# Performance work log

Measured on AMD Instinct MI355X. Metric: run time of the kernel, lower is better.

Reference implementation:

```python
import jax, jax.numpy as jnp
import numpy as np

B, S, H = 1, 2048, 2880
NH, HD = 64, 64            # num_attention_heads, head_dim
NKV = 8                    # num_key_value_heads
GROUPS = NH // NKV         # 8
RANK = 384                 # kv_lora_rank
ROPE_BASE = 150000.0
NEG = -3.4e38              # additive mask value (finfo min-ish)


def setup_inputs() -> dict:
    key = jax.random.key(0)
    ks = jax.random.split(key, 8)
    init = 0.02
    hidden_states = jax.random.normal(ks[0], (B, S, H), dtype=jnp.float32)
    # causal additive mask [B,1,S,S]
    causal = jnp.tril(jnp.ones((S, S), dtype=bool))
    attention_mask = jnp.where(causal, 0.0, NEG).astype(jnp.float32)[None, None]
    attention_mask = jnp.broadcast_to(attention_mask, (B, 1, S, S))
    q_w = jax.random.normal(ks[1], (NH * HD, H), dtype=jnp.float32) * init
    q_b = jnp.zeros((NH * HD,), dtype=jnp.float32)
    kv_a_w = jax.random.normal(ks[2], (RANK, H), dtype=jnp.float32) * init
    kv_b_w = jax.random.normal(ks[3], (NKV * HD * 2, RANK), dtype=jnp.float32) * init
    o_w = jax.random.normal(ks[4], (H, NH * HD), dtype=jnp.float32) * init
    o_b = jnp.zeros((H,), dtype=jnp.float32)
    return {"hidden_states": hidden_states, "attention_mask": attention_mask,
            "q_w": q_w, "q_b": q_b, "kv_a_w": kv_a_w, "kv_b_w": kv_b_w,
            "o_w": o_w, "o_b": o_b}


def _rotate_half(x):
    x1, x2 = x[..., : x.shape[-1] // 2], x[..., x.shape[-1] // 2:]
    return jnp.concatenate((-x2, x1), axis=-1)


def _rope_cos_sin(S, dtype):
    inv_freq = 1.0 / (ROPE_BASE ** (jnp.arange(0, HD, 2, dtype=jnp.float32) / HD))
    pos = jnp.arange(S, dtype=jnp.float32)
    freqs = pos[:, None] * inv_freq[None, :]          # [S, HD/2]
    emb = jnp.concatenate((freqs, freqs), axis=-1)    # [S, HD]
    # [1, 1, S, HD] to broadcast over batch and heads
    return jnp.cos(emb).astype(dtype)[None, None], jnp.sin(emb).astype(dtype)[None, None]


def reference(hidden_states, attention_mask, q_w, q_b, kv_a_w, kv_b_w, o_w, o_b):
    B, S, H = hidden_states.shape
    # Q projection -> [B, NH, S, HD]
    q = (hidden_states @ q_w.T + q_b).reshape(B, S, NH, HD).transpose(0, 2, 1, 3)
    # compressed KV -> decompress
    compressed_kv = hidden_states @ kv_a_w.T                 # [B, S, RANK]
    kv = (compressed_kv @ kv_b_w.T).reshape(B, S, NKV, 2 * HD)
    k, v = kv[..., :HD], kv[..., HD:]
    k = k.transpose(0, 2, 1, 3)                              # [B, NKV, S, HD]
    v = v.transpose(0, 2, 1, 3)
    # full-dim RoPE (module applies rotary over entire head_dim)
    cos, sin = _rope_cos_sin(S, q.dtype)
    q = q * cos + _rotate_half(q) * sin
    k = k * cos + _rotate_half(k) * sin
    # GQA expand: repeat_interleave over head axis
    k = jnp.repeat(k, GROUPS, axis=1)                        # [B, NH, S, HD]
    v = jnp.repeat(v, GROUPS, axis=1)
    scores = jnp.einsum('bhqd,bhkd->bhqk', q, k) / np.sqrt(HD)
    scores = scores + attention_mask
    probs = jax.nn.softmax(scores.astype(jnp.float32), axis=-1).astype(q.dtype)
    attn = jnp.einsum('bhqk,bhkd->bhqd', probs, v)           # [B, NH, S, HD]
    attn = attn.transpose(0, 2, 1, 3).reshape(B, S, NH * HD)
    return attn @ o_w.T + o_b
```

## Files before the change

### kernel.cpp

```cpp
#include <hip/hip_runtime.h>
#include <math.h>

typedef unsigned short u16;
typedef unsigned int u32;
typedef float f4 __attribute__((ext_vector_type(4)));
typedef short bf16x8 __attribute__((ext_vector_type(8)));
typedef float f32x4 __attribute__((ext_vector_type(4)));

#define S_LEN 2048
#define H_DIM 2880
#define NQD 4096
#define RANKD 384
#define HD 64
#define NH 64
#define NKV 8
#define RLN 0.37244970541f
#define LOG2E 1.4426950408889634f

__device__ __forceinline__ u16 f2bf(float f) {
  u32 u = __float_as_uint(f);
  u += 0x7fffu + ((u >> 16) & 1u);
  return (u16)(u >> 16);
}

#define GLOAD_LDS(g, l) __builtin_amdgcn_global_load_lds( \
    (__attribute__((address_space(1))) void*)(g),          \
    (__attribute__((address_space(3))) void*)(l), 16, 0, 0)

__device__ __forceinline__ size_t koff_s(int s) {
  return (size_t)((s >> 6) * 4096 + ((s >> 4) & 3) * 1024 + (s & 15) * 8);
}
__device__ __forceinline__ int koff_d(int d) {
  return (d >> 5) * 512 + ((d >> 3) & 3) * 128 + (d & 7);
}
__device__ __forceinline__ size_t voff_s(int s) {
  return (size_t)((s >> 6) * 4096 + ((s >> 5) & 1) * 512 + ((s >> 3) & 3) * 128 + (s & 7));
}
__device__ __forceinline__ int voff_d(int d) {
  return ((d >> 4) & 3) * 1024 + (d & 15) * 8;
}

__global__ void conv_f2b(const float* __restrict__ in, u16* __restrict__ out, int n4) {
  int i = blockIdx.x * blockDim.x + threadIdx.x;
  if (i >= n4) return;
  f4 v = ((const f4*)in)[i];
  ushort4 o;
  o.x = f2bf(v[0]); o.y = f2bf(v[1]); o.z = f2bf(v[2]); o.w = f2bf(v[3]);
  ((ushort4*)out)[i] = o;
}

__global__ __launch_bounds__(256) void gemm128(
    const u16* __restrict__ A, const u16* __restrict__ W,
    const float* __restrict__ bias, int K,
    u16* __restrict__ out0) {
  __shared__ __align__(16) u16 As[2 * 2 * 128 * 32];
  __shared__ __align__(16) u16 Bs[2 * 2 * 128 * 32];
  int t = threadIdx.x, w = t >> 6, L = t & 63;
  int lm = L & 15, quad = L >> 4;
  int m0 = blockIdx.x * 128, n0 = blockIdx.y * 128;
  int wm = w >> 1, wn = w & 1;
  int srow = L >> 2, scol8 = (L & 3) * 8;
  const u16* Ag0 = A + (size_t)(m0 + (w * 2) * 16 + srow) * K + scol8;
  const u16* Ag1 = Ag0 + (size_t)16 * K;
  const u16* Wg0 = W + (size_t)(n0 + (w * 2) * 16 + srow) * K + scol8;
  const u16* Wg1 = Wg0 + (size_t)16 * K;
  u16* lA0 = &As[(w * 2) * 512];
  u16* lA1 = &As[(w * 2 + 1) * 512];
  u16* lB0 = &Bs[(w * 2) * 512];
  u16* lB1 = &Bs[(w * 2 + 1) * 512];
  f32x4 acc[4][4] = {};
  int nk = K >> 6;
  GLOAD_LDS(Ag0, lA0);           GLOAD_LDS(Ag1, lA1);
  GLOAD_LDS(Ag0 + 32, lA0 + 4096); GLOAD_LDS(Ag1 + 32, lA1 + 4096);
  GLOAD_LDS(Wg0, lB0);           GLOAD_LDS(Wg1, lB1);
  GLOAD_LDS(Wg0 + 32, lB0 + 4096); GLOAD_LDS(Wg1 + 32, lB1 + 4096);
  Ag0 += 64; Ag1 += 64; Wg0 += 64; Wg1 += 64;
  __syncthreads();
  for (int kt = 0; kt < nk; ++kt) {
    int cur = (kt & 1) << 13;
    int nxt = 8192 - cur;
    if (kt + 1 < nk) {
      GLOAD_LDS(Ag0, lA0 + nxt);           GLOAD_LDS(Ag1, lA1 + nxt);
      GLOAD_LDS(Ag0 + 32, lA0 + nxt + 4096); GLOAD_LDS(Ag1 + 32, lA1 + nxt + 4096);
      GLOAD_LDS(Wg0, lB0 + nxt);           GLOAD_LDS(Wg1, lB1 + nxt);
      GLOAD_LDS(Wg0 + 32, lB0 + nxt + 4096); GLOAD_LDS(Wg1 + 32, lB1 + nxt + 4096);
      Ag0 += 64; Ag1 += 64; Wg0 += 64; Wg1 += 64;
    }
#pragma unroll
    for (int h = 0; h < 2; ++h) {
      int base = cur + h * 4096;
      bf16x8 af[4], bf[4];
#pragma unroll
      for (int i = 0; i < 4; ++i) af[i] = *(const bf16x8*)&As[base + (wm * 64 + i * 16 + lm) * 32 + quad * 8];
#pragma unroll
      for (int j = 0; j < 4; ++j) bf[j] = *(const bf16x8*)&Bs[base + (wn * 64 + j * 16 + lm) * 32 + quad * 8];
#pragma unroll
      for (int i = 0; i < 4; ++i)
#pragma unroll
        for (int j = 0; j < 4; ++j)
          acc[i][j] = __builtin_amdgcn_mfma_f32_16x16x32_bf16(af[i], bf[j], acc[i][j], 0, 0, 0);
    }
    __syncthreads();
  }
  int head = (n0 + wn * 64) >> 6;
  float b0v = bias[head * 64 + lm];
  float b1v = bias[head * 64 + 16 + lm];
  float b2v = bias[head * 64 + 32 + lm];
  float b3v = bias[head * 64 + 48 + lm];
  float invf1 = __expf(-(float)lm * RLN);
  float invf2 = __expf(-(float)(lm + 16) * RLN);
#pragma unroll
  for (int i = 0; i < 4; ++i) {
    int sq = m0 + wm * 64 + i * 16 + quad * 4;
#pragma unroll
    for (int r = 0; r < 4; ++r) {
      float a0 = acc[i][0][r] + b0v, a1 = acc[i][1][r] + b1v;
      float a2 = acc[i][2][r] + b2v, a3 = acc[i][3][r] + b3v;
      float s1, c1, s2, c2;
      sincosf((float)(sq + r) * invf1, &s1, &c1);
      sincosf((float)(sq + r) * invf2, &s2, &c2);
      u16* op = out0 + ((size_t)head * S_LEN + sq + r) * HD;
      op[lm]      = f2bf((a0 * c1 - a2 * s1) * 0.125f);
      op[lm + 32] = f2bf((a2 * c1 + a0 * s1) * 0.125f);
      op[lm + 16] = f2bf((a1 * c2 - a3 * s2) * 0.125f);
      op[lm + 48] = f2bf((a3 * c2 + a1 * s2) * 0.125f);
    }
  }
}

__global__ __launch_bounds__(256) void gemm64(
    const u16* __restrict__ A, const u16* __restrict__ W,
    const float* __restrict__ bias, int K, int Nreal,
    float* __restrict__ out) {
  __shared__ __align__(16) u16 As[2 * 2 * 64 * 32];
  __shared__ __align__(16) u16 Bs[2 * 2 * 128 * 32];
  int t = threadIdx.x, w = t >> 6, L = t & 63;
  int lm = L & 15, quad = L >> 4;
  int m0 = blockIdx.x * 64, n0 = blockIdx.y * 128;
  int wm = w >> 1, wn = w & 1;
  int srow = L >> 2, scol8 = (L & 3) * 8;
  const u16* Ag = A + (size_t)(m0 + w * 16 + srow) * K + scol8;
  int wr0 = n0 + w * 16 + srow;      if (wr0 > Nreal - 1) wr0 = Nreal - 1;
  int wr1 = n0 + 64 + w * 16 + srow; if (wr1 > Nreal - 1) wr1 = Nreal - 1;
  const u16* Wg0 = W + (size_t)wr0 * K + scol8;
  const u16* Wg1 = W + (size_t)wr1 * K + scol8;
  u16* lA  = &As[w * 512];
  u16* lB0 = &Bs[w * 512];
  u16* lB1 = &Bs[2048 + w * 512];
  f32x4 acc[2][4] = {};
  int nk = K >> 6;
  GLOAD_LDS(Ag, lA);            GLOAD_LDS(Ag + 32, lA + 2048);
  GLOAD_LDS(Wg0, lB0);          GLOAD_LDS(Wg0 + 32, lB0 + 4096);
  GLOAD_LDS(Wg1, lB1);          GLOAD_LDS(Wg1 + 32, lB1 + 4096);
  Ag += 64; Wg0 += 64; Wg1 += 64;
  __syncthreads();
  for (int kt = 0; kt < nk; ++kt) {
    int curA = (kt & 1) << 12;
    int curB = (kt & 1) << 13;
    int nxtA = 4096 - curA, nxtB = 8192 - curB;
    if (kt + 1 < nk) {
      GLOAD_LDS(Ag, lA + nxtA);          GLOAD_LDS(Ag + 32, lA + nxtA + 2048);
      GLOAD_LDS(Wg0, lB0 + nxtB);        GLOAD_LDS(Wg0 + 32, lB0 + nxtB + 4096);
      GLOAD_LDS(Wg1, lB1 + nxtB);        GLOAD_LDS(Wg1 + 32, lB1 + nxtB + 4096);
      Ag += 64; Wg0 += 64; Wg1 += 64;
    }
#pragma unroll
    for (int h = 0; h < 2; ++h) {
      int baseA = curA + h * 2048;
      int baseB = curB + h * 4096;
      bf16x8 af[2], bf[4];
#pragma unroll
      for (int i = 0; i < 2; ++i) af[i] = *(const bf16x8*)&As[baseA + (wm * 32 + i * 16 + lm) * 32 + quad * 8];
#pragma unroll
      for (int j = 0; j < 4; ++j) bf[j] = *(const bf16x8*)&Bs[baseB + (wn * 64 + j * 16 + lm) * 32 + quad * 8];
#pragma unroll
      for (int i = 0; i < 2; ++i)
#pragma unroll
        for (int j = 0; j < 4; ++j)
          acc[i][j] = __builtin_amdgcn_mfma_f32_16x16x32_bf16(af[i], bf[j], acc[i][j], 0, 0, 0);
    }
    __syncthreads();
  }
#pragma unroll
  for (int i = 0; i < 2; ++i) {
#pragma unroll
    for (int r = 0; r < 4; ++r) {
      int row = m0 + wm * 32 + i * 16 + quad * 4 + r;
#pragma unroll
      for (int j = 0; j < 4; ++j) {
        int col = n0 + wn * 64 + j * 16 + lm;
        if (col < Nreal)
          out[(size_t)row * Nreal + col] = acc[i][j][r] + bias[col];
      }
    }
  }
}

__global__ __launch_bounds__(256) void gemm_bt(
    const u16* __restrict__ A, const u16* __restrict__ W,
    int M, int N, int K, int mode,
    u16* __restrict__ out0, u16* __restrict__ out1) {
  __shared__ __align__(16) u16 As[64 * 32];
  __shared__ __align__(16) u16 Bs[64 * 32];
  int t = threadIdx.x;
  int m0 = blockIdx.x * 64, n0 = blockIdx.y * 64;
  int w = t >> 6, L = t & 63;
  int srow = t >> 2, scol = (t & 3) * 8;
  int lm = L & 15, quad = L >> 4;
  const u16* Ap = A + (size_t)(m0 + srow) * K + scol;
  const u16* Wp = W + (size_t)(n0 + srow) * K + scol;
  f32x4 acc0 = {0.f, 0.f, 0.f, 0.f}, acc1 = acc0, acc2 = acc0, acc3 = acc0;
  int aoff = (w * 16 + lm) * 32 + quad * 8;
  int boff = lm * 32 + quad * 8;
  int nk = K >> 5;
  uint4 av = *(const uint4*)Ap;
  uint4 wv = *(const uint4*)Wp;
  for (int kt = 0; kt < nk; ++kt) {
    *(uint4*)&As[srow * 32 + scol] = av;
    *(uint4*)&Bs[srow * 32 + scol] = wv;
    __syncthreads();
    if (kt + 1 < nk) {
      Ap += 32; Wp += 32;
      av = *(const uint4*)Ap;
      wv = *(const uint4*)Wp;
    }
    bf16x8 af = *(const bf16x8*)&As[aoff];
    bf16x8 b0 = *(const bf16x8*)&Bs[boff];
    bf16x8 b1 = *(const bf16x8*)&Bs[boff + 16 * 32];
    bf16x8 b2 = *(const bf16x8*)&Bs[boff + 32 * 32];
    bf16x8 b3 = *(const bf16x8*)&Bs[boff + 48 * 32];
    acc0 = __builtin_amdgcn_mfma_f32_16x16x32_bf16(af, b0, acc0, 0, 0, 0);
    acc1 = __builtin_amdgcn_mfma_f32_16x16x32_bf16(af, b1, acc1, 0, 0, 0);
    acc2 = __builtin_amdgcn_mfma_f32_16x16x32_bf16(af, b2, acc2, 0, 0, 0);
    acc3 = __builtin_amdgcn_mfma_f32_16x16x32_bf16(af, b3, acc3, 0, 0, 0);
    __syncthreads();
  }
  int mbase = m0 + w * 16 + quad * 4;
  if (mode == 3) {
    for (int r = 0; r < 4; ++r) {
      int row = mbase + r;
      float vals[4] = {acc0[r], acc1[r], acc2[r], acc3[r]};
      for (int nt = 0; nt < 4; ++nt)
        out0[(size_t)row * N + (n0 + nt * 16 + lm)] = f2bf(vals[nt]);
    }
  } else {
    bool isV = ((blockIdx.y & 1) == 1);
    int head = (n0 >> 7);
    size_t hb = (size_t)head << 17;
    if (isV) {
      int dof[4];
#pragma unroll
      for (int nt = 0; nt < 4; ++nt) dof[nt] = voff_d(nt * 16 + lm);
      for (int r = 0; r < 4; ++r) {
        int s = mbase + r;
        size_t so = hb + voff_s(s);
        float vals[4] = {acc0[r], acc1[r], acc2[r], acc3[r]};
#pragma unroll
        for (int nt = 0; nt < 4; ++nt)
          out1[so + dof[nt]] = f2bf(vals[nt]);
      }
    } else {
      int d0 = koff_d(lm), d1 = koff_d(lm + 16), d2 = koff_d(lm + 32), d3 = koff_d(lm + 48);
      float invf1 = __expf(-(float)lm * RLN);
      float invf2 = __expf(-(float)(lm + 16) * RLN);
      for (int r = 0; r < 4; ++r) {
        int s = mbase + r;
        float a0 = acc0[r], a1 = acc1[r], a2 = acc2[r], a3 = acc3[r];
        float s1, c1, s2, c2;
        sincosf((float)s * invf1, &s1, &c1);
        sincosf((float)s * invf2, &s2, &c2);
        s1 *= LOG2E; c1 *= LOG2E; s2 *= LOG2E; c2 *= LOG2E;
        size_t so = hb + koff_s(s);
        out0[so + d0] = f2bf(a0 * c1 - a2 * s1);
        out0[so + d2] = f2bf(a2 * c1 + a0 * s1);
        out0[so + d1] = f2bf(a1 * c2 - a3 * s2);
        out0[so + d3] = f2bf(a3 * c2 + a1 * s2);
      }
    }
  }
}

__global__ __launch_bounds__(256, 4) void attn_v3(
    const u16* __restrict__ Qb, const u16* __restrict__ Kf,
    const u16* __restrict__ Vf, u16* __restrict__ attnb) {
  __shared__ __align__(16) u16 Ps[4 * 16 * 72];
  int t = threadIdx.x;
  int w = t >> 6, L = t & 63;
  int lm = L & 15, quad = L >> 4;
  int h = blockIdx.x, qt = blockIdx.y, kvh = h >> 3;
  u16* pw = &Ps[w * 16 * 72];
  const u16* Kbase = Kf + ((size_t)kvh << 17) + L * 8;
  const u16* Vbase = Vf + ((size_t)kvh << 17) + L * 8;

  int q0 = qt * 64;
  const u16* Qp = Qb + ((size_t)h * S_LEN + q0 + w * 16 + lm) * HD + quad * 8;
  bf16x8 qf0 = *(const bf16x8*)Qp;
  bf16x8 qf1 = *(const bf16x8*)(Qp + 32);
  f32x4 o[4] = {};
  float m_ = -3.0e38f, l_ = 0.f;

  for (int c = 0; c <= qt; ++c) {
    const u16* Kc = Kbase + (size_t)c * 4096;
    bf16x8 kfa[4], kfb[4];
#pragma unroll
    for (int j = 0; j < 4; ++j) {
      kfa[j] = *(const bf16x8*)(Kc + j * 1024);
      kfb[j] = *(const bf16x8*)(Kc + j * 1024 + 512);
    }
    f32x4 st[4] = {};
    __builtin_amdgcn_s_setprio(1);
#pragma unroll
    for (int j = 0; j < 4; ++j) {
      st[j] = __builtin_amdgcn_mfma_f32_16x16x32_bf16(kfa[j], qf0, st[j], 0, 0, 0);
      st[j] = __builtin_amdgcn_mfma_f32_16x16x32_bf16(kfb[j], qf1, st[j], 0, 0, 0);
    }
    __builtin_amdgcn_s_setprio(0);
    const u16* Vc = Vbase + (size_t)c * 4096;
    bf16x8 vfa[4], vfb[4];
#pragma unroll
    for (int j = 0; j < 4; ++j) {
      vfa[j] = *(const bf16x8*)(Vc + j * 1024);
      vfb[j] = *(const bf16x8*)(Vc + j * 1024 + 512);
    }
    if (c == qt) {
      int qloc = w * 16 + lm;
#pragma unroll
      for (int j = 0; j < 4; ++j) {
        int kvb = j * 16 + quad * 4;
#pragma unroll
        for (int r = 0; r < 4; ++r)
          if (kvb + r > qloc) st[j][r] = -3.0e38f;
      }
    }
    float mloc = -3.0e38f;
#pragma unroll
    for (int j = 0; j < 4; ++j)
      mloc = fmaxf(mloc, fmaxf(fmaxf(st[j][0], st[j][1]), fmaxf(st[j][2], st[j][3])));
    mloc = fmaxf(mloc, __shfl_xor(mloc, 16));
    mloc = fmaxf(mloc, __shfl_xor(mloc, 32));
    float mn;
    if (__all(mloc - m_ <= 11.0f)) {
      mn = m_;
    } else {
      mn = fmaxf(m_, mloc);
      float al = exp2f(m_ - mn);
      m_ = mn;
      l_ *= al;
      float a0 = __shfl(al, quad * 4 + 0);
      float a1 = __shfl(al, quad * 4 + 1);
      float a2 = __shfl(al, quad * 4 + 2);
      float a3 = __shfl(al, quad * 4 + 3);
#pragma unroll
      for (int j = 0; j < 4; ++j) {
        o[j][0] *= a0; o[j][1] *= a1; o[j][2] *= a2; o[j][3] *= a3;
      }
    }
    float sum = 0.f;
    u16* pws = pw + lm * 72;
#pragma unroll
    for (int j = 0; j < 4; ++j) {
      float p0 = exp2f(st[j][0] - mn);
      float p1 = exp2f(st[j][1] - mn);
      float p2 = exp2f(st[j][2] - mn);
      float p3 = exp2f(st[j][3] - mn);
      sum += (p0 + p1) + (p2 + p3);
      uint2 pk;
      asm("v_cvt_pk_bf16_f32 %0, %1, %2" : "=v"(pk.x) : "v"(p0), "v"(p1));
      asm("v_cvt_pk_bf16_f32 %0, %1, %2" : "=v"(pk.y) : "v"(p2), "v"(p3));
      *(uint2*)(pws + j * 16 + quad * 4) = pk;
    }
    l_ += sum;
    bf16x8 pa = *(const bf16x8*)(pw + lm * 72 + quad * 8);
    bf16x8 pb = *(const bf16x8*)(pw + lm * 72 + 32 + quad * 8);
    __builtin_amdgcn_s_setprio(1);
#pragma unroll
    for (int j = 0; j < 4; ++j) {
      o[j] = __builtin_amdgcn_mfma_f32_16x16x32_bf16(pa, vfa[j], o[j], 0, 0, 0);
      o[j] = __builtin_amdgcn_mfma_f32_16x16x32_bf16(pb, vfb[j], o[j], 0, 0, 0);
    }
    __builtin_amdgcn_s_setprio(0);
  }
  l_ += __shfl_xor(l_, 16);
  l_ += __shfl_xor(l_, 32);
  float linv = 1.0f / l_;
  float li0 = __shfl(linv, quad * 4 + 0);
  float li1 = __shfl(linv, quad * 4 + 1);
  float li2 = __shfl(linv, quad * 4 + 2);
  float li3 = __shfl(linv, quad * 4 + 3);
#pragma unroll
  for (int r = 0; r < 4; ++r) {
    float lr = (r == 0) ? li0 : (r == 1) ? li1 : (r == 2) ? li2 : li3;
    int row = q0 + w * 16 + quad * 4 + r;
    u16* op = attnb + (size_t)row * NQD + h * HD;
    op[lm]      = f2bf(o[0][r] * lr);
    op[lm + 16] = f2bf(o[1][r] * lr);
    op[lm + 32] = f2bf(o[2][r] * lr);
    op[lm + 48] = f2bf(o[3][r] * lr);
  }
}

extern "C" void kernel_launch(void* const* d_in, const int* in_sizes, int n_in,
                              void* d_out, int out_size, void* d_ws, size_t ws_size,
                              hipStream_t stream) {
  (void)in_sizes; (void)n_in; (void)out_size; (void)ws_size;
  const float* hidden = (const float*)d_in[0];
  const float* q_w    = (const float*)d_in[2];
  const float* q_b    = (const float*)d_in[3];
  const float* kv_a_w = (const float*)d_in[4];
  const float* kv_b_w = (const float*)d_in[5];
  const float* o_w    = (const float*)d_in[6];
  const float* o_b    = (const float*)d_in[7];

  char* ws = (char*)d_ws;
  u16* hb    = (u16*)(ws + 0);
  u16* qwb   = (u16*)(ws + 11796480);
  u16* kab   = (u16*)(ws + 35389440);
  u16* kbb   = (u16*)(ws + 37601280);
  u16* owb   = (u16*)(ws + 38387712);
  u16* Qb    = (u16*)(ws + 61980672);
  u16* CKVb  = (u16*)(ws + 78757888);
  u16* Kfb   = (u16*)(ws + 80330752);
  u16* Vfb   = (u16*)(ws + 82427904);
  u16* attnb = (u16*)(ws + 84525056);

  conv_f2b<<<(1474560 + 255) / 256, 256, 0, stream>>>(hidden, hb, 1474560);
  conv_f2b<<<(2949120 + 255) / 256, 256, 0, stream>>>(q_w, qwb, 2949120);
  conv_f2b<<<(276480 + 255) / 256, 256, 0, stream>>>(kv_a_w, kab, 276480);
  conv_f2b<<<(98304 + 255) / 256, 256, 0, stream>>>(kv_b_w, kbb, 98304);
  conv_f2b<<<(2949120 + 255) / 256, 256, 0, stream>>>(o_w, owb, 2949120);

  gemm128<<<dim3(16, 32), 256, 0, stream>>>(hb, qwb, q_b, H_DIM, Qb);
  gemm_bt<<<dim3(32, 6),  256, 0, stream>>>(hb, kab, S_LEN, RANKD, H_DIM, 3, CKVb, nullptr);
  gemm_bt<<<dim3(32, 16), 256, 0, stream>>>(CKVb, kbb, S_LEN, 1024, RANKD, 2, Kfb, Vfb);
  attn_v3<<<dim3(64, 32), 256, 0, stream>>>(Qb, Kfb, Vfb, attnb);
  gemm64<<<dim3(32, 23), 256, 0, stream>>>(attnb, owb, o_b, NQD, H_DIM, (float*)d_out);
}
```

Baseline: 417.7 us.

## Pair causal q-tiles per attention block and double-buffer gemm_bt via direct LDS loads

The attention kernel now processes two query tiles per block, qt and 31-qt, so every block gets a roughly equal amount of causal work, and the grid is halved. The small projection GEMM switches to global-to-LDS direct loads with a double-buffered 64-wide K step, to hide load latency and cut VGPR staging. The trade-offs are fewer blocks in flight for attention and reliance on the async LDS loads being complete at each barrier.

```diff
diff --git a/kernel.cpp b/kernel.cpp
--- a/kernel.cpp
+++ b/kernel.cpp
@@ -200,39 +200,46 @@
     const u16* __restrict__ A, const u16* __restrict__ W,
     int M, int N, int K, int mode,
     u16* __restrict__ out0, u16* __restrict__ out1) {
-  __shared__ __align__(16) u16 As[64 * 32];
-  __shared__ __align__(16) u16 Bs[64 * 32];
+  __shared__ __align__(16) u16 As[2 * 2 * 64 * 32];
+  __shared__ __align__(16) u16 Bs[2 * 2 * 64 * 32];
   int t = threadIdx.x;
   int m0 = blockIdx.x * 64, n0 = blockIdx.y * 64;
   int w = t >> 6, L = t & 63;
-  int srow = t >> 2, scol = (t & 3) * 8;
   int lm = L & 15, quad = L >> 4;
-  const u16* Ap = A + (size_t)(m0 + srow) * K + scol;
-  const u16* Wp = W + (size_t)(n0 + srow) * K + scol;
+  int srow = w * 16 + (L >> 2), scol = (L & 3) * 8;
+  const u16* Ag = A + (size_t)(m0 + srow) * K + scol;
+  const u16* Wg = W + (size_t)(n0 + srow) * K + scol;
+  u16* lA = &As[w * 512];
+  u16* lB = &Bs[w * 512];
   f32x4 acc0 = {0.f, 0.f, 0.f, 0.f}, acc1 = acc0, acc2 = acc0, acc3 = acc0;
   int aoff = (w * 16 + lm) * 32 + quad * 8;
   int boff = lm * 32 + quad * 8;
-  int nk = K >> 5;
-  uint4 av = *(const uint4*)Ap;
-  uint4 wv = *(const uint4*)Wp;
+  int nk = K >> 6;
+  GLOAD_LDS(Ag, lA);       GLOAD_LDS(Ag + 32, lA + 2048);
+  GLOAD_LDS(Wg, lB);       GLOAD_LDS(Wg + 32, lB + 2048);
+  Ag += 64; Wg += 64;
+  __syncthreads();
   for (int kt = 0; kt < nk; ++kt) {
-    *(uint4*)&As[srow * 32 + scol] = av;
-    *(uint4*)&Bs[srow * 32 + scol] = wv;
-    __syncthreads();
+    int cur = (kt & 1) << 12;
+    int nxt = 4096 - cur;
     if (kt + 1 < nk) {
-      Ap += 32; Wp += 32;
-      av = *(const uint4*)Ap;
-      wv = *(const uint4*)Wp;
-    }
-    bf16x8 af = *(const bf16x8*)&As[aoff];
-    bf16x8 b0 = *(const bf16x8*)&Bs[boff];
-    bf16x8 b1 = *(const bf16x8*)&Bs[boff + 16 * 32];
-    bf16x8 b2 = *(const bf16x8*)&Bs[boff + 32 * 32];
-    bf16x8 b3 = *(const bf16x8*)&Bs[boff + 48 * 32];
-    acc0 = __builtin_amdgcn_mfma_f32_16x16x32_bf16(af, b0, acc0, 0, 0, 0);
-    acc1 = __builtin_amdgcn_mfma_f32_16x16x32_bf16(af, b1, acc1, 0, 0, 0);
-    acc2 = __builtin_amdgcn_mfma_f32_16x16x32_bf16(af, b2, acc2, 0, 0, 0);
-    acc3 = __builtin_amdgcn_mfma_f32_16x16x32_bf16(af, b3, acc3, 0, 0, 0);
+      GLOAD_LDS(Ag, lA + nxt);   GLOAD_LDS(Ag + 32, lA + nxt + 2048);
+      GLOAD_LDS(Wg, lB + nxt);   GLOAD_LDS(Wg + 32, lB + nxt + 2048);
+      Ag += 64; Wg += 64;
+    }
+#pragma unroll
+    for (int hh = 0; hh < 2; ++hh) {
+      int base = cur + hh * 2048;
+      bf16x8 af = *(const bf16x8*)&As[base + aoff];
+      bf16x8 b0 = *(const bf16x8*)&Bs[base + boff];
+      bf16x8 b1 = *(const bf16x8*)&Bs[base + boff + 16 * 32];
+      bf16x8 b2 = *(const bf16x8*)&Bs[base + boff + 32 * 32];
+      bf16x8 b3 = *(const bf16x8*)&Bs[base + boff + 48 * 32];
+      acc0 = __builtin_amdgcn_mfma_f32_16x16x32_bf16(af, b0, acc0, 0, 0, 0);
+      acc1 = __builtin_amdgcn_mfma_f32_16x16x32_bf16(af, b1, acc1, 0, 0, 0);
+      acc2 = __builtin_amdgcn_mfma_f32_16x16x32_bf16(af, b2, acc2, 0, 0, 0);
+      acc3 = __builtin_amdgcn_mfma_f32_16x16x32_bf16(af, b3, acc3, 0, 0, 0);
+    }
     __syncthreads();
   }
   int mbase = m0 + w * 16 + quad * 4;
@@ -287,115 +294,118 @@
   int t = threadIdx.x;
   int w = t >> 6, L = t & 63;
   int lm = L & 15, quad = L >> 4;
-  int h = blockIdx.x, qt = blockIdx.y, kvh = h >> 3;
+  int bx = blockIdx.x, h = blockIdx.y, kvh = h >> 3;
   u16* pw = &Ps[w * 16 * 72];
   const u16* Kbase = Kf + ((size_t)kvh << 17) + L * 8;
   const u16* Vbase = Vf + ((size_t)kvh << 17) + L * 8;
 
-  int q0 = qt * 64;
-  const u16* Qp = Qb + ((size_t)h * S_LEN + q0 + w * 16 + lm) * HD + quad * 8;
-  bf16x8 qf0 = *(const bf16x8*)Qp;
-  bf16x8 qf1 = *(const bf16x8*)(Qp + 32);
-  f32x4 o[4] = {};
-  float m_ = -3.0e38f, l_ = 0.f;
-
-  for (int c = 0; c <= qt; ++c) {
-    const u16* Kc = Kbase + (size_t)c * 4096;
-    bf16x8 kfa[4], kfb[4];
-#pragma unroll
-    for (int j = 0; j < 4; ++j) {
-      kfa[j] = *(const bf16x8*)(Kc + j * 1024);
-      kfb[j] = *(const bf16x8*)(Kc + j * 1024 + 512);
-    }
-    f32x4 st[4] = {};
-    __builtin_amdgcn_s_setprio(1);
-#pragma unroll
-    for (int j = 0; j < 4; ++j) {
-      st[j] = __builtin_amdgcn_mfma_f32_16x16x32_bf16(kfa[j], qf0, st[j], 0, 0, 0);
-      st[j] = __builtin_amdgcn_mfma_f32_16x16x32_bf16(kfb[j], qf1, st[j], 0, 0, 0);
-    }
-    __builtin_amdgcn_s_setprio(0);
-    const u16* Vc = Vbase + (size_t)c * 4096;
-    bf16x8 vfa[4], vfb[4];
-#pragma unroll
-    for (int j = 0; j < 4; ++j) {
-      vfa[j] = *(const bf16x8*)(Vc + j * 1024);
-      vfb[j] = *(const bf16x8*)(Vc + j * 1024 + 512);
-    }
-    if (c == qt) {
-      int qloc = w * 16 + lm;
-#pragma unroll
-      for (int j = 0; j < 4; ++j) {
-        int kvb = j * 16 + quad * 4;
-#pragma unroll
-        for (int r = 0; r < 4; ++r)
-          if (kvb + r > qloc) st[j][r] = -3.0e38f;
-      }
-    }
-    float mloc = -3.0e38f;
-#pragma unroll
-    for (int j = 0; j < 4; ++j)
-      mloc = fmaxf(mloc, fmaxf(fmaxf(st[j][0], st[j][1]), fmaxf(st[j][2], st[j][3])));
-    mloc = fmaxf(mloc, __shfl_xor(mloc, 16));
-    mloc = fmaxf(mloc, __shfl_xor(mloc, 32));
-    float mn;
-    if (__all(mloc - m_ <= 11.0f)) {
-      mn = m_;
-    } else {
-      mn = fmaxf(m_, mloc);
-      float al = exp2f(m_ - mn);
-      m_ = mn;
-      l_ *= al;
-      float a0 = __shfl(al, quad * 4 + 0);
-      float a1 = __shfl(al, quad * 4 + 1);
-      float a2 = __shfl(al, quad * 4 + 2);
-      float a3 = __shfl(al, quad * 4 + 3);
-#pragma unroll
-      for (int j = 0; j < 4; ++j) {
-        o[j][0] *= a0; o[j][1] *= a1; o[j][2] *= a2; o[j][3] *= a3;
-      }
-    }
-    float sum = 0.f;
-    u16* pws = pw + lm * 72;
-#pragma unroll
-    for (int j = 0; j < 4; ++j) {
-      float p0 = exp2f(st[j][0] - mn);
-      float p1 = exp2f(st[j][1] - mn);
-      float p2 = exp2f(st[j][2] - mn);
-      float p3 = exp2f(st[j][3] - mn);
-      sum += (p0 + p1) + (p2 + p3);
-      uint2 pk;
-      asm("v_cvt_pk_bf16_f32 %0, %1, %2" : "=v"(pk.x) : "v"(p0), "v"(p1));
-      asm("v_cvt_pk_bf16_f32 %0, %1, %2" : "=v"(pk.y) : "v"(p2), "v"(p3));
-      *(uint2*)(pws + j * 16 + quad * 4) = pk;
-    }
-    l_ += sum;
-    bf16x8 pa = *(const bf16x8*)(pw + lm * 72 + quad * 8);
-    bf16x8 pb = *(const bf16x8*)(pw + lm * 72 + 32 + quad * 8);
-    __builtin_amdgcn_s_setprio(1);
-#pragma unroll
-    for (int j = 0; j < 4; ++j) {
-      o[j] = __builtin_amdgcn_mfma_f32_16x16x32_bf16(pa, vfa[j], o[j], 0, 0, 0);
-      o[j] = __builtin_amdgcn_mfma_f32_16x16x32_bf16(pb, vfb[j], o[j], 0, 0, 0);
-    }
-    __builtin_amdgcn_s_setprio(0);
-  }
-  l_ += __shfl_xor(l_, 16);
-  l_ += __shfl_xor(l_, 32);
-  float linv = 1.0f / l_;
-  float li0 = __shfl(linv, quad * 4 + 0);
-  float li1 = __shfl(linv, quad * 4 + 1);
-  float li2 = __shfl(linv, quad * 4 + 2);
-  float li3 = __shfl(linv, quad * 4 + 3);
-#pragma unroll
-  for (int r = 0; r < 4; ++r) {
-    float lr = (r == 0) ? li0 : (r == 1) ? li1 : (r == 2) ? li2 : li3;
-    int row = q0 + w * 16 + quad * 4 + r;
-    u16* op = attnb + (size_t)row * NQD + h * HD;
-    op[lm]      = f2bf(o[0][r] * lr);
-    op[lm + 16] = f2bf(o[1][r] * lr);
-    op[lm + 32] = f2bf(o[2][r] * lr);
-    op[lm + 48] = f2bf(o[3][r] * lr);
+  for (int ph = 0; ph < 2; ++ph) {
+    int qt = ph ? (31 - bx) : bx;
+    int q0 = qt * 64;
+    const u16* Qp = Qb + ((size_t)h * S_LEN + q0 + w * 16 + lm) * HD + quad * 8;
+    bf16x8 qf0 = *(const bf16x8*)Qp;
+    bf16x8 qf1 = *(const bf16x8*)(Qp + 32);
+    f32x4 o[4] = {};
+    float m_ = -3.0e38f, l_ = 0.f;
+
+    for (int c = 0; c <= qt; ++c) {
+      const u16* Kc = Kbase + (size_t)c * 4096;
+      bf16x8 kfa[4], kfb[4];
+#pragma unroll
+      for (int j = 0; j < 4; ++j) {
+        kfa[j] = *(const bf16x8*)(Kc + j * 1024);
+        kfb[j] = *(const bf16x8*)(Kc + j * 1024 + 512);
+      }
+      f32x4 st[4] = {};
+      __builtin_amdgcn_s_setprio(1);
+#pragma unroll
+      for (int j = 0; j < 4; ++j) {
+        st[j] = __builtin_amdgcn_mfma_f32_16x16x32_bf16(kfa[j], qf0, st[j], 0, 0, 0);
+        st[j] = __builtin_amdgcn_mfma_f32_16x16x32_bf16(kfb[j], qf1, st[j], 0, 0, 0);
+      }
+      __builtin_amdgcn_s_setprio(0);
+      const u16* Vc = Vbase + (size_t)c * 4096;
+      bf16x8 vfa[4], vfb[4];
+#pragma unroll
+      for (int j = 0; j < 4; ++j) {
+        vfa[j] = *(const bf16x8*)(Vc + j * 1024);
+        vfb[j] = *(const bf16x8*)(Vc + j * 1024 + 512);
+      }
+      if (c == qt) {
+        int qloc = w * 16 + lm;
+#pragma unroll
+        for (int j = 0; j < 4; ++j) {
+          int kvb = j * 16 + quad * 4;
+#pragma unroll
+          for (int r = 0; r < 4; ++r)
+            if (kvb + r > qloc) st[j][r] = -3.0e38f;
+        }
+      }
+      float mloc = -3.0e38f;
+#pragma unroll
+      for (int j = 0; j < 4; ++j)
+        mloc = fmaxf(mloc, fmaxf(fmaxf(st[j][0], st[j][1]), fmaxf(st[j][2], st[j][3])));
+      mloc = fmaxf(mloc, __shfl_xor(mloc, 16));
+      mloc = fmaxf(mloc, __shfl_xor(mloc, 32));
+      float mn;
+      if (__all(mloc - m_ <= 11.0f)) {
+        mn = m_;
+      } else {
+        mn = fmaxf(m_, mloc);
+        float al = exp2f(m_ - mn);
+        m_ = mn;
+        l_ *= al;
+        float a0 = __shfl(al, quad * 4 + 0);
+        float a1 = __shfl(al, quad * 4 + 1);
+        float a2 = __shfl(al, quad * 4 + 2);
+        float a3 = __shfl(al, quad * 4 + 3);
+#pragma unroll
+        for (int j = 0; j < 4; ++j) {
+          o[j][0] *= a0; o[j][1] *= a1; o[j][2] *= a2; o[j][3] *= a3;
+        }
+      }
+      float sum = 0.f;
+      u16* pws = pw + lm * 72;
+#pragma unroll
+      for (int j = 0; j < 4; ++j) {
+        float p0 = exp2f(st[j][0] - mn);
+        float p1 = exp2f(st[j][1] - mn);
+        float p2 = exp2f(st[j][2] - mn);
+        float p3 = exp2f(st[j][3] - mn);
+        sum += (p0 + p1) + (p2 + p3);
+        uint2 pk;
+        asm("v_cvt_pk_bf16_f32 %0, %1, %2" : "=v"(pk.x) : "v"(p0), "v"(p1));
+        asm("v_cvt_pk_bf16_f32 %0, %1, %2" : "=v"(pk.y) : "v"(p2), "v"(p3));
+        *(uint2*)(pws + j * 16 + quad * 4) = pk;
+      }
+      l_ += sum;
+      bf16x8 pa = *(const bf16x8*)(pw + lm * 72 + quad * 8);
+      bf16x8 pb = *(const bf16x8*)(pw + lm * 72 + 32 + quad * 8);
+      __builtin_amdgcn_s_setprio(1);
+#pragma unroll
+      for (int j = 0; j < 4; ++j) {
+        o[j] = __builtin_amdgcn_mfma_f32_16x16x32_bf16(pa, vfa[j], o[j], 0, 0, 0);
+        o[j] = __builtin_amdgcn_mfma_f32_16x16x32_bf16(pb, vfb[j], o[j], 0, 0, 0);
+      }
+      __builtin_amdgcn_s_setprio(0);
+    }
+    l_ += __shfl_xor(l_, 16);
+    l_ += __shfl_xor(l_, 32);
+    float linv = 1.0f / l_;
+    float li0 = __shfl(linv, quad * 4 + 0);
+    float li1 = __shfl(linv, quad * 4 + 1);
+    float li2 = __shfl(linv, quad * 4 + 2);
+    float li3 = __shfl(linv, quad * 4 + 3);
+#pragma unroll
+    for (int r = 0; r < 4; ++r) {
+      float lr = (r == 0) ? li0 : (r == 1) ? li1 : (r == 2) ? li2 : li3;
+      int row = q0 + w * 16 + quad * 4 + r;
+      u16* op = attnb + (size_t)row * NQD + h * HD;
+      op[lm]      = f2bf(o[0][r] * lr);
+      op[lm + 16] = f2bf(o[1][r] * lr);
+      op[lm + 32] = f2bf(o[2][r] * lr);
+      op[lm + 48] = f2bf(o[3][r] * lr);
+    }
   }
 }
 
@@ -432,6 +442,6 @@
   gemm128<<<dim3(16, 32), 256, 0, stream>>>(hb, qwb, q_b, H_DIM, Qb);
   gemm_bt<<<dim3(32, 6),  256, 0, stream>>>(hb, kab, S_LEN, RANKD, H_DIM, 3, CKVb, nullptr);
   gemm_bt<<<dim3(32, 16), 256, 0, stream>>>(CKVb, kbb, S_LEN, 1024, RANKD, 2, Kfb, Vfb);
-  attn_v3<<<dim3(64, 32), 256, 0, stream>>>(Qb, Kfb, Vfb, attnb);
+  attn_v3<<<dim3(16, 64), 256, 0, stream>>>(Qb, Kfb, Vfb, attnb);
   gemm64<<<dim3(32, 23), 256, 0, stream>>>(attnb, owb, o_b, NQD, H_DIM, (float*)d_out);
 }
```

Measured after the change: 418.5 us. Within noise of the previous version (+0.2%).
